# Performance work log

Measured on AMD Instinct MI355X. Metric: run time of the kernel, lower is better.

Reference implementation:

```python
import jax, jax.numpy as jnp
import numpy as np

B, N, DIM = 4, 2048, 128
HEADS, HEAD = 8, 128
INNER = HEADS * HEAD  # 1024
EPS = 1e-5


def setup_inputs() -> dict:
    key = jax.random.key(0)
    k0, k1, k2 = jax.random.split(key, 3)
    return {
        "x": jax.random.normal(k0, (B, N, DIM), jnp.float32),
        "ln_gamma": jnp.ones((DIM,), jnp.float32),
        "ln_beta": jnp.zeros((DIM,), jnp.float32),
        "w_qkv": jax.random.normal(k1, (3 * INNER, DIM), jnp.float32) * (DIM ** -0.5),
        "w_out": jax.random.normal(k2, (DIM, INNER), jnp.float32) * (INNER ** -0.5),
        "b_out": jnp.zeros((DIM,), jnp.float32),
    }


def _rope(t):
    """lucidrains-style rotary embedding over full last dim of t: [b,h,n,d]."""
    n, d = t.shape[-2], t.shape[-1]
    inv_freq = 1.0 / (10000.0 ** (jnp.arange(0, d, 2, dtype=jnp.float32) / d))
    freqs = jnp.arange(n, dtype=jnp.float32)[:, None] * inv_freq[None, :]  # [n, d/2]
    freqs = jnp.repeat(freqs, 2, axis=-1)  # interleaved duplicate -> [n, d]
    cos, sin = jnp.cos(freqs), jnp.sin(freqs)
    # rotate_half on interleaved pairs: (x1, x2) -> (-x2, x1)
    x1, x2 = t[..., 0::2], t[..., 1::2]
    rot = jnp.stack((-x2, x1), axis=-1).reshape(t.shape)
    return t * cos + rot * sin


def reference(x, ln_gamma, ln_beta, w_qkv, w_out, b_out):
    # LayerNorm
    mu = x.mean(-1, keepdims=True)
    var = x.var(-1, keepdims=True)
    xn = (x - mu) * jax.lax.rsqrt(var + EPS) * ln_gamma + ln_beta
    # QKV projection (bias-free)
    qkv = jnp.einsum('bnd,ed->bne', xn, w_qkv)  # [B, N, 3*INNER]
    q, k, v = jnp.split(qkv, 3, axis=-1)
    to_heads = lambda t: t.reshape(B, N, HEADS, HEAD).transpose(0, 2, 1, 3)
    q, k, v = to_heads(q), to_heads(k), to_heads(v)  # [B, H, N, HEAD]
    # Partial RoPE: rotate all but the last token; last token stays unrotated
    q = jnp.concatenate([_rope(q[:, :, :-1]), q[:, :, -1:]], axis=2)
    k = jnp.concatenate([_rope(k[:, :, :-1]), k[:, :, -1:]], axis=2)
    scale = HEAD ** -0.5
    dots = jnp.einsum('bhid,bhjd->bhij', q, k) * scale  # [B, H, N, N]
    attn = jax.nn.softmax(dots, axis=-1)
    out = jnp.einsum('bhij,bhjd->bhid', attn, v)
    out = out.transpose(0, 2, 1, 3).reshape(B, N, INNER)
    return out @ w_out.T + b_out
```

## Files before the change

kernel.cpp:

```cpp
#include <hip/hip_runtime.h>
#include <hip/hip_bf16.h>
#include <hip/hip_fp16.h>

#define B_      4
#define N_      2048
#define DIM_    128
#define HEADS_  8
#define HEAD_   128
#define INNER_  1024
#define QKV_    3072
#define EPS_    1e-5f
#define SCALE_  0.08838834764831845f
#define ROPE_C  0.20762050593046015f

typedef __attribute__((ext_vector_type(8))) short short8;
typedef __attribute__((ext_vector_type(4))) short short4v;
typedef __attribute__((ext_vector_type(4))) float f32x4;


__device__ __forceinline__ unsigned short f2bf(float f) {
    unsigned u = __builtin_bit_cast(unsigned, f);
    u = (u + 0x7fffu + ((u >> 16) & 1u)) >> 16;
    return (unsigned short)u;
}
__device__ __forceinline__ float bf2f(unsigned short h) {
    unsigned u = ((unsigned)h) << 16;
    return __builtin_bit_cast(float, u);
}
__device__ __forceinline__ unsigned pk2(float a, float b) {
    return (unsigned)f2bf(a) | ((unsigned)f2bf(b) << 16);
}
__device__ __forceinline__ short4v pack4(const float* e) {
    __hip_bfloat162 h0 = __float22bfloat162_rn(make_float2(e[0], e[1]));
    __hip_bfloat162 h1 = __float22bfloat162_rn(make_float2(e[2], e[3]));
    uint2 u;
    __builtin_memcpy(&u.x, &h0, 4);
    __builtin_memcpy(&u.y, &h1, 4);
    return __builtin_bit_cast(short4v, u);
}

__device__ __forceinline__ int kidx(int r, int chunk) {
    return r * 128 + ((chunk ^ (r & 7)) << 3);
}
__device__ __forceinline__ int vidx(int r, int chunk) {
    return r * 64 + ((chunk ^ (r & 7)) << 3);
}

__global__ __launch_bounds__(256) void k_ln(
    const float* __restrict__ x, const float* __restrict__ g,
    const float* __restrict__ be, unsigned short* __restrict__ xnb)
{
    const int w = threadIdx.x >> 6, l = threadIdx.x & 63;
    const int row = blockIdx.x * 4 + w;
    float2 v = *(const float2*)(x + (size_t)row * 128 + l * 2);
    float s = v.x + v.y, s2 = v.x * v.x + v.y * v.y;
#pragma unroll
    for (int off = 1; off < 64; off <<= 1) {
        s  += __shfl_xor(s, off);
        s2 += __shfl_xor(s2, off);
    }
    float mu = s * (1.f / 128.f);
    float var = s2 * (1.f / 128.f) - mu * mu;
    float rs = rsqrtf(var + EPS_);
    float2 gg = *(const float2*)(g + l * 2);
    float2 bb = *(const float2*)(be + l * 2);
    float ox = (v.x - mu) * rs * gg.x + bb.x;
    float oy = (v.y - mu) * rs * gg.y + bb.y;
    *(unsigned*)(xnb + (size_t)row * 128 + l * 2) = pk2(ox, oy);
}

__global__ __launch_bounds__(256) void k_cvt(
    const float* __restrict__ src, unsigned short* __restrict__ dst)
{
    size_t i = ((size_t)blockIdx.x * 256 + threadIdx.x) * 8;
    float4 f0 = *(const float4*)(src + i), f1 = *(const float4*)(src + i + 4);
    uint4 u = { pk2(f0.x, f0.y), pk2(f0.z, f0.w), pk2(f1.x, f1.y), pk2(f1.z, f1.w) };
    *(uint4*)(dst + i) = u;
}

__global__ __launch_bounds__(256) void k_qkvf(
    const unsigned short* __restrict__ xnb, const unsigned short* __restrict__ wb,
    unsigned short* __restrict__ Q, unsigned short* __restrict__ K,
    unsigned short* __restrict__ Vt)
{
    __shared__ unsigned short lA[128 * 136];
    __shared__ unsigned short lB[128 * 136];
    const int t = threadIdx.x;
    const int wv = t >> 6, l = t & 63;
    const int lm = l & 15, quad = l >> 4;
    const int row0 = blockIdx.x * 128;
    const int by   = blockIdx.y;
    const int e0   = by * 128;

#pragma unroll
    for (int i = 0; i < 8; ++i) {
        int c = t + 256 * i;  int r = c >> 4, c8 = c & 15;
        *(uint4*)&lA[r * 136 + c8 * 8] =
            *(const uint4*)(xnb + (size_t)(row0 + r) * 128 + c8 * 8);
        *(uint4*)&lB[r * 136 + c8 * 8] =
            *(const uint4*)(wb + (size_t)(e0 + r) * 128 + c8 * 8);
    }
    __syncthreads();

    short8 af[2][4];
#pragma unroll
    for (int mt = 0; mt < 2; ++mt)
#pragma unroll
        for (int ks = 0; ks < 4; ++ks)
            af[mt][ks] = *(short8*)&lA[(wv * 32 + mt * 16 + lm) * 136 + ks * 32 + quad * 8];

    f32x4 acc[2][8];
#pragma unroll
    for (int mt = 0; mt < 2; ++mt)
#pragma unroll
        for (int ct = 0; ct < 8; ++ct) acc[mt][ct] = (f32x4){0.f, 0.f, 0.f, 0.f};
#pragma unroll
    for (int ks = 0; ks < 4; ++ks) {
#pragma unroll
        for (int ct = 0; ct < 8; ++ct) {
            short8 b = *(short8*)&lB[(ct * 16 + lm) * 136 + ks * 32 + quad * 8];
            acc[0][ct] = __builtin_amdgcn_mfma_f32_16x16x32_bf16(af[0][ks], b, acc[0][ct], 0, 0, 0);
            acc[1][ct] = __builtin_amdgcn_mfma_f32_16x16x32_bf16(af[1][ks], b, acc[1][ct], 0, 0, 0);
        }
    }
    __syncthreads();

    const int b  = row0 >> 11;
    const int n0 = row0 & (N_ - 1);
    const int h  = by & 7;
    const int bh = b * 8 + h;

    if (by < 16) {
#pragma unroll
        for (int mt = 0; mt < 2; ++mt)
#pragma unroll
            for (int ct = 0; ct < 8; ++ct)
#pragma unroll
                for (int r = 0; r < 4; ++r)
                    lA[(wv * 32 + mt * 16 + quad * 4 + r) * 136 + ct * 16 + lm] =
                        f2bf(acc[mt][ct][r]);
        __syncthreads();

        const int r_loc = t >> 1, half = t & 1;
        const int n = n0 + r_loc;
        unsigned short* dst = (by < 8 ? Q : K) +
            ((size_t)bh * N_ + n) * HEAD_ + half * 64;
        const bool dorope = (n != N_ - 1);
#pragma unroll
        for (int j = 0; j < 8; ++j) {
            short8 vv = *(short8*)&lA[r_loc * 136 + half * 64 + j * 8];
            if (dorope) {
                unsigned short* pv = (unsigned short*)&vv;
#pragma unroll
                for (int p = 0; p < 4; ++p) {
                    int i0 = half * 32 + j * 4 + p;
                    float invf = exp2f(-(float)i0 * ROPE_C);
                    float th = (float)n * invf;
                    float cs = __cosf(th), sn = __sinf(th);
                    float e = bf2f(pv[2 * p]), o = bf2f(pv[2 * p + 1]);
                    pv[2 * p]     = f2bf(e * cs - o * sn);
                    pv[2 * p + 1] = f2bf(o * cs + e * sn);
                }
            }
            *(short8*)(dst + j * 8) = vv;
        }
    } else {
#pragma unroll
        for (int mt = 0; mt < 2; ++mt)
#pragma unroll
            for (int ct = 0; ct < 8; ++ct)
#pragma unroll
                for (int r = 0; r < 4; ++r)
                    lA[(ct * 16 + lm) * 136 + wv * 32 + quad * 8 + mt * 4 + r] =
                        f2bf(acc[mt][ct][r]);
        __syncthreads();

        const int d = t >> 1, half = t & 1;
        unsigned short* dst = Vt + ((size_t)bh * HEAD_ + d) * N_ + n0 + half * 64;
#pragma unroll
        for (int j = 0; j < 8; ++j)
            *(short8*)(dst + j * 8) = *(short8*)&lA[d * 136 + half * 64 + j * 8];
    }
}

__global__ __launch_bounds__(256) void k_attn(
    const unsigned short* __restrict__ Q, const unsigned short* __restrict__ K,
    const unsigned short* __restrict__ Vt, unsigned short* __restrict__ Ob)
{
    __shared__ unsigned short lK[64 * 128];
    __shared__ unsigned short lV[128 * 64];

    const int t = threadIdx.x;
    const int w = t >> 6, l = t & 63;
    const int lm = l & 15, quad = l >> 4;
    const int bid = blockIdx.x;
    const int bh = bid & 31;
    const int qt = bid >> 5;
    const int n0 = qt * 128;
    const unsigned short* Qb = Q  + (size_t)bh * N_ * HEAD_;
    const unsigned short* Kb = K  + (size_t)bh * N_ * HEAD_;
    const unsigned short* Vb = Vt + (size_t)bh * N_ * HEAD_;

    short8 aq[2][4];
#pragma unroll
    for (int tt = 0; tt < 2; ++tt) {
        const unsigned short* qp =
            Qb + ((size_t)(n0 + tt * 64 + w * 16 + lm)) * 128 + quad * 8;
#pragma unroll
        for (int ks = 0; ks < 4; ++ks)
            aq[tt][ks] = *(const short8*)(qp + ks * 32);
    }

    f32x4 Oa[2][8];
#pragma unroll
    for (int tt = 0; tt < 2; ++tt)
#pragma unroll
        for (int i = 0; i < 8; ++i) Oa[tt][i] = (f32x4){0.f, 0.f, 0.f, 0.f};
    float ps0 = 0.f, ps1 = 0.f;
    const float C1 = SCALE_ * 1.44269504f;
    const float C0 = -23.08312f;

    short8 kr[4], vr[4];
#pragma unroll
    for (int i = 0; i < 4; ++i) {
        int c = t + 256 * i;
        kr[i] = *(const short8*)(Kb + ((size_t)(c >> 4)) * 128 + (c & 15) * 8);
        vr[i] = *(const short8*)(Vb + (size_t)(c >> 3) * N_ + (c & 7) * 8);
    }

    for (int jt = 0; jt < 32; ++jt) {
        __syncthreads();
#pragma unroll
        for (int i = 0; i < 4; ++i) {
            int c = t + 256 * i;
            *(short8*)&lK[kidx(c >> 4, c & 15)] = kr[i];
            *(short8*)&lV[vidx(c >> 3, c & 7)]  = vr[i];
        }
        __syncthreads();
        if (jt < 31) {
#pragma unroll
            for (int i = 0; i < 4; ++i) {
                int c = t + 256 * i;
                kr[i] = *(const short8*)(Kb + ((size_t)((jt + 1) * 64 + (c >> 4))) * 128 + (c & 15) * 8);
                vr[i] = *(const short8*)(Vb + (size_t)(c >> 3) * N_ + (jt + 1) * 64 + (c & 7) * 8);
            }
        }

        short4v pf0[4], pf1[4];
#pragma unroll
        for (int nb = 0; nb < 4; ++nb) {
            f32x4 st0 = (f32x4){0.f, 0.f, 0.f, 0.f};
            f32x4 st1 = (f32x4){0.f, 0.f, 0.f, 0.f};
#pragma unroll
            for (int ks = 0; ks < 4; ++ks) {
                short8 kf = *(short8*)&lK[kidx(nb * 16 + lm, (ks << 2) + quad)];
                st0 = __builtin_amdgcn_mfma_f32_16x16x32_bf16(kf, aq[0][ks], st0, 0, 0, 0);
                st1 = __builtin_amdgcn_mfma_f32_16x16x32_bf16(kf, aq[1][ks], st1, 0, 0, 0);
            }
            float e0[4], e1[4];
#pragma unroll
            for (int r = 0; r < 4; ++r) {
                e0[r] = exp2f(st0[r] * C1 + C0);
                e1[r] = exp2f(st1[r] * C1 + C0);
                ps0 += e0[r];  ps1 += e1[r];
            }
            pf0[nb] = pack4(e0);
            pf1[nb] = pack4(e1);
        }

#pragma unroll
        for (int c2 = 0; c2 < 2; ++c2) {
            short8 ap0 = __builtin_shufflevector(pf0[2 * c2], pf0[2 * c2 + 1],
                                                 0, 1, 2, 3, 4, 5, 6, 7);
            short8 ap1 = __builtin_shufflevector(pf1[2 * c2], pf1[2 * c2 + 1],
                                                 0, 1, 2, 3, 4, 5, 6, 7);
#pragma unroll
            for (int nb8 = 0; nb8 < 8; ++nb8) {
                short8 bv = *(short8*)&lV[vidx(nb8 * 16 + lm, (c2 << 2) + quad)];
                Oa[0][nb8] = __builtin_amdgcn_mfma_f32_16x16x32_bf16(ap0, bv, Oa[0][nb8], 0, 0, 0);
                Oa[1][nb8] = __builtin_amdgcn_mfma_f32_16x16x32_bf16(ap1, bv, Oa[1][nb8], 0, 0, 0);
            }
        }
    }

    ps0 += __shfl_xor(ps0, 16);  ps0 += __shfl_xor(ps0, 32);
    ps1 += __shfl_xor(ps1, 16);  ps1 += __shfl_xor(ps1, 32);

    const int b = bh >> 3, h = bh & 7;
#pragma unroll
    for (int tt = 0; tt < 2; ++tt)
#pragma unroll
        for (int r = 0; r < 4; ++r) {
            float lsum = __shfl(tt == 0 ? ps0 : ps1, (l & 48) | (quad * 4 + r));
            float il = 1.f / lsum;
            int n = n0 + tt * 64 + w * 16 + quad * 4 + r;
            unsigned short* op = Ob + ((size_t)b * N_ + n) * INNER_ + h * HEAD_ + lm;
#pragma unroll
            for (int nb8 = 0; nb8 < 8; ++nb8)
                op[nb8 * 16] = f2bf(Oa[tt][nb8][r] * il);
        }
}

__global__ __launch_bounds__(256) void k_attn2(
    const unsigned short* __restrict__ Q, const unsigned short* __restrict__ K,
    const unsigned short* __restrict__ Vt, float* __restrict__ Opart,
    float* __restrict__ psb)
{
    __shared__ unsigned short lK[64 * 128];
    __shared__ unsigned short lV[128 * 64];

    const int t = threadIdx.x;
    const int w = t >> 6, l = t & 63;
    const int lm = l & 15, quad = l >> 4;
    const int bid = blockIdx.x;
    const int s   = bid >> 9;
    const int p   = bid & 511;
    const int bh  = bid & 31;
    const int qt  = (bid >> 5) & 15;
    const int n0  = qt * 128;
    const int jt0 = s * 16;
    const unsigned short* Qb = Q  + (size_t)bh * N_ * HEAD_;
    const unsigned short* Kb = K  + (size_t)bh * N_ * HEAD_;
    const unsigned short* Vb = Vt + (size_t)bh * N_ * HEAD_;

    short8 aq[2][4];
#pragma unroll
    for (int tt = 0; tt < 2; ++tt) {
        const unsigned short* qp =
            Qb + ((size_t)(n0 + tt * 64 + w * 16 + lm)) * 128 + quad * 8;
#pragma unroll
        for (int ks = 0; ks < 4; ++ks)
            aq[tt][ks] = *(const short8*)(qp + ks * 32);
    }

    f32x4 Oa[2][8];
#pragma unroll
    for (int tt = 0; tt < 2; ++tt)
#pragma unroll
        for (int i = 0; i < 8; ++i) Oa[tt][i] = (f32x4){0.f, 0.f, 0.f, 0.f};
    float ps0 = 0.f, ps1 = 0.f;
    const float C1 = SCALE_ * 1.44269504f;
    const float C0 = -23.08312f;

    short8 kr[4], vr[4];
#pragma unroll
    for (int i = 0; i < 4; ++i) {
        int c = t + 256 * i;
        kr[i] = *(const short8*)(Kb + ((size_t)(jt0 * 64 + (c >> 4))) * 128 + (c & 15) * 8);
        vr[i] = *(const short8*)(Vb + (size_t)(c >> 3) * N_ + jt0 * 64 + (c & 7) * 8);
    }

    for (int jt = 0; jt < 16; ++jt) {
        __syncthreads();
#pragma unroll
        for (int i = 0; i < 4; ++i) {
            int c = t + 256 * i;
            *(short8*)&lK[kidx(c >> 4, c & 15)] = kr[i];
            *(short8*)&lV[vidx(c >> 3, c & 7)]  = vr[i];
        }
        __syncthreads();
        if (jt < 15) {
#pragma unroll
            for (int i = 0; i < 4; ++i) {
                int c = t + 256 * i;
                kr[i] = *(const short8*)(Kb + ((size_t)((jt0 + jt + 1) * 64 + (c >> 4))) * 128 + (c & 15) * 8);
                vr[i] = *(const short8*)(Vb + (size_t)(c >> 3) * N_ + (jt0 + jt + 1) * 64 + (c & 7) * 8);
            }
        }

        short4v pf0[4], pf1[4];
#pragma unroll
        for (int nb = 0; nb < 4; ++nb) {
            f32x4 st0 = (f32x4){0.f, 0.f, 0.f, 0.f};
            f32x4 st1 = (f32x4){0.f, 0.f, 0.f, 0.f};
#pragma unroll
            for (int ks = 0; ks < 4; ++ks) {
                short8 kf = *(short8*)&lK[kidx(nb * 16 + lm, (ks << 2) + quad)];
                st0 = __builtin_amdgcn_mfma_f32_16x16x32_bf16(kf, aq[0][ks], st0, 0, 0, 0);
                st1 = __builtin_amdgcn_mfma_f32_16x16x32_bf16(kf, aq[1][ks], st1, 0, 0, 0);
            }
            float e0[4], e1[4];
#pragma unroll
            for (int r = 0; r < 4; ++r) {
                e0[r] = exp2f(st0[r] * C1 + C0);
                e1[r] = exp2f(st1[r] * C1 + C0);
                ps0 += e0[r];  ps1 += e1[r];
            }
            pf0[nb] = pack4(e0);
            pf1[nb] = pack4(e1);
        }

#pragma unroll
        for (int c2 = 0; c2 < 2; ++c2) {
            short8 ap0 = __builtin_shufflevector(pf0[2 * c2], pf0[2 * c2 + 1],
                                                 0, 1, 2, 3, 4, 5, 6, 7);
            short8 ap1 = __builtin_shufflevector(pf1[2 * c2], pf1[2 * c2 + 1],
                                                 0, 1, 2, 3, 4, 5, 6, 7);
#pragma unroll
            for (int nb8 = 0; nb8 < 8; ++nb8) {
                short8 bv = *(short8*)&lV[vidx(nb8 * 16 + lm, (c2 << 2) + quad)];
                Oa[0][nb8] = __builtin_amdgcn_mfma_f32_16x16x32_bf16(ap0, bv, Oa[0][nb8], 0, 0, 0);
                Oa[1][nb8] = __builtin_amdgcn_mfma_f32_16x16x32_bf16(ap1, bv, Oa[1][nb8], 0, 0, 0);
            }
        }
    }

    ps0 += __shfl_xor(ps0, 16);  ps0 += __shfl_xor(ps0, 32);
    ps1 += __shfl_xor(ps1, 16);  ps1 += __shfl_xor(ps1, 32);

    float* Op = Opart + ((size_t)(s * 512 + p)) * 16384;
    float* pp = psb   + ((size_t)(s * 512 + p)) * 128;
#pragma unroll
    for (int tt = 0; tt < 2; ++tt)
#pragma unroll
        for (int r = 0; r < 4; ++r) {
            float lsum = __shfl(tt == 0 ? ps0 : ps1, (l & 48) | (quad * 4 + r));
            int rowl = tt * 64 + w * 16 + quad * 4 + r;
            if (lm == 0) pp[rowl] = lsum;
#pragma unroll
            for (int nb8 = 0; nb8 < 8; ++nb8)
                Op[rowl * 128 + nb8 * 16 + lm] = Oa[tt][nb8][r];
        }
}

__global__ __launch_bounds__(256) void k_comb(
    const float* __restrict__ Opart, const float* __restrict__ psb,
    unsigned short* __restrict__ Ob)
{
    __shared__ float inv[128];
    const int p = blockIdx.x;
    const int t = threadIdx.x;
    const int bh = p & 31, qt = p >> 5;
    if (t < 128) {
        float d = psb[(size_t)p * 128 + t] + psb[(size_t)(512 + p) * 128 + t];
        inv[t] = 1.f / d;
    }
    __syncthreads();
    const float* O0 = Opart + (size_t)p * 16384;
    const float* O1 = Opart + (size_t)(512 + p) * 16384;
    const int b = bh >> 3, h = bh & 7;
#pragma unroll
    for (int i = 0; i < 16; ++i) {
        int flat = i * 256 + t;
        int row = flat >> 5, dq = (flat & 31) * 4;
        float4 a = *(const float4*)(O0 + row * 128 + dq);
        float4 c = *(const float4*)(O1 + row * 128 + dq);
        float iv = inv[row];
        float e[4] = { (a.x + c.x) * iv, (a.y + c.y) * iv,
                       (a.z + c.z) * iv, (a.w + c.w) * iv };
        short4v o = pack4(e);
        int n = qt * 128 + row;
        *(short4v*)(Ob + ((size_t)b * N_ + n) * INNER_ + h * HEAD_ + dq) = o;
    }
}

__global__ __launch_bounds__(256) void k_proj(
    const unsigned short* __restrict__ Ob, const unsigned short* __restrict__ wob,
    const float* __restrict__ bias, float* __restrict__ out)
{
    __shared__ unsigned short lA[64 * 136];
    __shared__ unsigned short lB[64 * 136];
    float* lCf = (float*)lA;
    const int t = threadIdx.x;
    const int wv = t >> 6, l = t & 63;
    const int lm = l & 15, quad = l >> 4;
    const int row0 = blockIdx.x * 64;
    const int e0   = blockIdx.y * 64;

    f32x4 acc[4];
#pragma unroll
    for (int ct = 0; ct < 4; ++ct) acc[ct] = (f32x4){0.f, 0.f, 0.f, 0.f};

    for (int kt = 0; kt < 8; ++kt) {
        __syncthreads();
#pragma unroll
        for (int i = 0; i < 4; ++i) {
            int c = t + 256 * i;  int r = c >> 4, c8 = c & 15;
            *(uint4*)&lA[r * 136 + c8 * 8] =
                *(const uint4*)(Ob + (size_t)(row0 + r) * 1024 + kt * 128 + c8 * 8);
            *(uint4*)&lB[r * 136 + c8 * 8] =
                *(const uint4*)(wob + (size_t)(e0 + r) * 1024 + kt * 128 + c8 * 8);
        }
        __syncthreads();
        short8 a_[4];
#pragma unroll
        for (int ks = 0; ks < 4; ++ks)
            a_[ks] = *(short8*)&lA[(wv * 16 + lm) * 136 + ks * 32 + quad * 8];
#pragma unroll
        for (int ks = 0; ks < 4; ++ks)
#pragma unroll
            for (int ct = 0; ct < 4; ++ct) {
                short8 b = *(short8*)&lB[(ct * 16 + lm) * 136 + ks * 32 + quad * 8];
                acc[ct] = __builtin_amdgcn_mfma_f32_16x16x32_bf16(a_[ks], b, acc[ct], 0, 0, 0);
            }
    }
    __syncthreads();
#pragma unroll
    for (int ct = 0; ct < 4; ++ct)
#pragma unroll
        for (int r = 0; r < 4; ++r)
            lCf[(wv * 16 + quad * 4 + r) * 68 + ct * 16 + lm] = acc[ct][r];
    __syncthreads();
#pragma unroll
    for (int i = 0; i < 4; ++i) {
        int c = t + 256 * i;  int r = c >> 4, c4 = c & 15;
        float4 v = *(float4*)&lCf[r * 68 + c4 * 4];
        float4 b4 = *(const float4*)(bias + e0 + c4 * 4);
        v.x += b4.x; v.y += b4.y; v.z += b4.z; v.w += b4.w;
        *(float4*)(out + (size_t)(row0 + r) * 128 + e0 + c4 * 4) = v;
    }
}

extern "C" void kernel_launch(void* const* d_in, const int* in_sizes, int n_in,
                              void* d_out, int out_size, void* d_ws, size_t ws_size,
                              hipStream_t stream) {
    const float* x      = (const float*)d_in[0];
    const float* gamma  = (const float*)d_in[1];
    const float* beta   = (const float*)d_in[2];
    const float* w_qkv  = (const float*)d_in[3];
    const float* w_out  = (const float*)d_in[4];
    const float* b_out  = (const float*)d_in[5];
    float* out = (float*)d_out;
    char* wsb = (char*)d_ws;
    unsigned short* Q    = (unsigned short*)(wsb);
    unsigned short* K    = (unsigned short*)(wsb + (16ull << 20));
    unsigned short* Vt   = (unsigned short*)(wsb + (32ull << 20));
    unsigned short* Ob   = (unsigned short*)(wsb + (48ull << 20));
    unsigned short* xnb  = (unsigned short*)(wsb + (96ull << 20));
    unsigned short* wqb  = (unsigned short*)(wsb + (98ull << 20));
    unsigned short* wob  = (unsigned short*)(wsb + (99ull << 20));

    k_ln       <<<dim3(2048),    256, 0, stream>>>(x, gamma, beta, xnb);
    k_cvt      <<<dim3(192),     256, 0, stream>>>(w_qkv, wqb);
    k_cvt      <<<dim3(64),      256, 0, stream>>>(w_out, wob);
    k_qkvf     <<<dim3(64, 24),  256, 0, stream>>>(xnb, wqb, Q, K, Vt);

    if (ws_size >= (165ull << 20)) {
        float* Opart = (float*)(wsb + (100ull << 20));
        float* psb   = (float*)(wsb + (164ull << 20));
        k_attn2 <<<dim3(1024), 256, 0, stream>>>(Q, K, Vt, Opart, psb);
        k_comb  <<<dim3(512),  256, 0, stream>>>(Opart, psb, Ob);
    } else {
        k_attn  <<<dim3(512),  256, 0, stream>>>(Q, K, Vt, Ob);
    }
    k_proj     <<<dim3(128, 2),  256, 0, stream>>>(Ob, wob, b_out, out);
}
```

Baseline: 208.1 us.

## Fuse prep kernels, shrink qkv LDS, retile projection, add attn2 occupancy hint

```diff
diff --git a/kernel.cpp b/kernel.cpp
--- a/kernel.cpp
+++ b/kernel.cpp
@@ -46,36 +46,42 @@
     return r * 64 + ((chunk ^ (r & 7)) << 3);
 }
 
-__global__ __launch_bounds__(256) void k_ln(
+__global__ __launch_bounds__(256) void k_prep(
     const float* __restrict__ x, const float* __restrict__ g,
-    const float* __restrict__ be, unsigned short* __restrict__ xnb)
+    const float* __restrict__ be, const float* __restrict__ w_qkv,
+    const float* __restrict__ w_out, unsigned short* __restrict__ xnb,
+    unsigned short* __restrict__ wqb, unsigned short* __restrict__ wob)
 {
-    const int w = threadIdx.x >> 6, l = threadIdx.x & 63;
-    const int row = blockIdx.x * 4 + w;
-    float2 v = *(const float2*)(x + (size_t)row * 128 + l * 2);
-    float s = v.x + v.y, s2 = v.x * v.x + v.y * v.y;
-#pragma unroll
-    for (int off = 1; off < 64; off <<= 1) {
-        s  += __shfl_xor(s, off);
-        s2 += __shfl_xor(s2, off);
-    }
-    float mu = s * (1.f / 128.f);
-    float var = s2 * (1.f / 128.f) - mu * mu;
-    float rs = rsqrtf(var + EPS_);
-    float2 gg = *(const float2*)(g + l * 2);
-    float2 bb = *(const float2*)(be + l * 2);
-    float ox = (v.x - mu) * rs * gg.x + bb.x;
-    float oy = (v.y - mu) * rs * gg.y + bb.y;
-    *(unsigned*)(xnb + (size_t)row * 128 + l * 2) = pk2(ox, oy);
-}
-
-__global__ __launch_bounds__(256) void k_cvt(
-    const float* __restrict__ src, unsigned short* __restrict__ dst)
-{
-    size_t i = ((size_t)blockIdx.x * 256 + threadIdx.x) * 8;
-    float4 f0 = *(const float4*)(src + i), f1 = *(const float4*)(src + i + 4);
-    uint4 u = { pk2(f0.x, f0.y), pk2(f0.z, f0.w), pk2(f1.x, f1.y), pk2(f1.z, f1.w) };
-    *(uint4*)(dst + i) = u;
+    const int bid = blockIdx.x;
+    if (bid < 2048) {
+        const int w = threadIdx.x >> 6, l = threadIdx.x & 63;
+        const int row = bid * 4 + w;
+        float2 v = *(const float2*)(x + (size_t)row * 128 + l * 2);
+        float s = v.x + v.y, s2 = v.x * v.x + v.y * v.y;
+#pragma unroll
+        for (int off = 1; off < 64; off <<= 1) {
+            s  += __shfl_xor(s, off);
+            s2 += __shfl_xor(s2, off);
+        }
+        float mu = s * (1.f / 128.f);
+        float var = s2 * (1.f / 128.f) - mu * mu;
+        float rs = rsqrtf(var + EPS_);
+        float2 gg = *(const float2*)(g + l * 2);
+        float2 bb = *(const float2*)(be + l * 2);
+        float ox = (v.x - mu) * rs * gg.x + bb.x;
+        float oy = (v.y - mu) * rs * gg.y + bb.y;
+        *(unsigned*)(xnb + (size_t)row * 128 + l * 2) = pk2(ox, oy);
+    } else if (bid < 2240) {
+        size_t i = ((size_t)(bid - 2048) * 256 + threadIdx.x) * 8;
+        float4 f0 = *(const float4*)(w_qkv + i), f1 = *(const float4*)(w_qkv + i + 4);
+        uint4 u = { pk2(f0.x, f0.y), pk2(f0.z, f0.w), pk2(f1.x, f1.y), pk2(f1.z, f1.w) };
+        *(uint4*)(wqb + i) = u;
+    } else {
+        size_t i = ((size_t)(bid - 2240) * 256 + threadIdx.x) * 8;
+        float4 f0 = *(const float4*)(w_out + i), f1 = *(const float4*)(w_out + i + 4);
+        uint4 u = { pk2(f0.x, f0.y), pk2(f0.z, f0.w), pk2(f1.x, f1.y), pk2(f1.z, f1.w) };
+        *(uint4*)(wob + i) = u;
+    }
 }
 
 __global__ __launch_bounds__(256) void k_qkvf(
@@ -83,8 +89,7 @@
     unsigned short* __restrict__ Q, unsigned short* __restrict__ K,
     unsigned short* __restrict__ Vt)
 {
-    __shared__ unsigned short lA[128 * 136];
-    __shared__ unsigned short lB[128 * 136];
+    __shared__ unsigned short lB[128 * 128];
     const int t = threadIdx.x;
     const int wv = t >> 6, l = t & 63;
     const int lm = l & 15, quad = l >> 4;
@@ -92,33 +97,33 @@
     const int by   = blockIdx.y;
     const int e0   = by * 128;
 
+    short8 af[2][4];
+#pragma unroll
+    for (int mt = 0; mt < 2; ++mt)
+#pragma unroll
+        for (int ks = 0; ks < 4; ++ks)
+            af[mt][ks] = *(const short8*)(
+                xnb + (size_t)(row0 + wv * 32 + mt * 16 + lm) * 128 + ks * 32 + quad * 8);
+
 #pragma unroll
     for (int i = 0; i < 8; ++i) {
         int c = t + 256 * i;  int r = c >> 4, c8 = c & 15;
-        *(uint4*)&lA[r * 136 + c8 * 8] =
-            *(const uint4*)(xnb + (size_t)(row0 + r) * 128 + c8 * 8);
-        *(uint4*)&lB[r * 136 + c8 * 8] =
+        *(uint4*)&lB[r * 128 + ((c8 ^ (r & 7)) << 3)] =
             *(const uint4*)(wb + (size_t)(e0 + r) * 128 + c8 * 8);
     }
     __syncthreads();
 
-    short8 af[2][4];
+    f32x4 acc[2][8];
 #pragma unroll
     for (int mt = 0; mt < 2; ++mt)
 #pragma unroll
-        for (int ks = 0; ks < 4; ++ks)
-            af[mt][ks] = *(short8*)&lA[(wv * 32 + mt * 16 + lm) * 136 + ks * 32 + quad * 8];
-
-    f32x4 acc[2][8];
-#pragma unroll
-    for (int mt = 0; mt < 2; ++mt)
-#pragma unroll
         for (int ct = 0; ct < 8; ++ct) acc[mt][ct] = (f32x4){0.f, 0.f, 0.f, 0.f};
 #pragma unroll
     for (int ks = 0; ks < 4; ++ks) {
 #pragma unroll
         for (int ct = 0; ct < 8; ++ct) {
-            short8 b = *(short8*)&lB[(ct * 16 + lm) * 136 + ks * 32 + quad * 8];
+            int r = ct * 16 + lm;
+            short8 b = *(short8*)&lB[r * 128 + (((ks * 4 + quad) ^ (r & 7)) << 3)];
             acc[0][ct] = __builtin_amdgcn_mfma_f32_16x16x32_bf16(af[0][ks], b, acc[0][ct], 0, 0, 0);
             acc[1][ct] = __builtin_amdgcn_mfma_f32_16x16x32_bf16(af[1][ks], b, acc[1][ct], 0, 0, 0);
         }
@@ -136,9 +141,12 @@
 #pragma unroll
             for (int ct = 0; ct < 8; ++ct)
 #pragma unroll
-                for (int r = 0; r < 4; ++r)
-                    lA[(wv * 32 + mt * 16 + quad * 4 + r) * 136 + ct * 16 + lm] =
+                for (int r = 0; r < 4; ++r) {
+                    int row = wv * 32 + mt * 16 + quad * 4 + r;
+                    int chunk = ct * 2 + (lm >> 3);
+                    lB[row * 128 + ((chunk ^ (row & 7)) << 3) + (lm & 7)] =
                         f2bf(acc[mt][ct][r]);
+                }
         __syncthreads();
 
         const int r_loc = t >> 1, half = t & 1;
@@ -148,7 +156,7 @@
         const bool dorope = (n != N_ - 1);
 #pragma unroll
         for (int j = 0; j < 8; ++j) {
-            short8 vv = *(short8*)&lA[r_loc * 136 + half * 64 + j * 8];
+            short8 vv = *(short8*)&lB[r_loc * 128 + (((half * 8 + j) ^ (r_loc & 7)) << 3)];
             if (dorope) {
                 unsigned short* pv = (unsigned short*)&vv;
 #pragma unroll
@@ -170,16 +178,20 @@
 #pragma unroll
             for (int ct = 0; ct < 8; ++ct)
 #pragma unroll
-                for (int r = 0; r < 4; ++r)
-                    lA[(ct * 16 + lm) * 136 + wv * 32 + quad * 8 + mt * 4 + r] =
+                for (int r = 0; r < 4; ++r) {
+                    int row = ct * 16 + lm;
+                    int chunk = wv * 4 + quad;
+                    lB[row * 128 + ((chunk ^ (row & 7)) << 3) + mt * 4 + r] =
                         f2bf(acc[mt][ct][r]);
+                }
         __syncthreads();
 
         const int d = t >> 1, half = t & 1;
         unsigned short* dst = Vt + ((size_t)bh * HEAD_ + d) * N_ + n0 + half * 64;
 #pragma unroll
         for (int j = 0; j < 8; ++j)
-            *(short8*)(dst + j * 8) = *(short8*)&lA[d * 136 + half * 64 + j * 8];
+            *(short8*)(dst + j * 8) =
+                *(short8*)&lB[d * 128 + (((half * 8 + j) ^ (d & 7)) << 3)];
     }
 }
 
@@ -187,8 +199,8 @@
     const unsigned short* __restrict__ Q, const unsigned short* __restrict__ K,
     const unsigned short* __restrict__ Vt, unsigned short* __restrict__ Ob)
 {
-    __shared__ unsigned short lK[64 * 128];
-    __shared__ unsigned short lV[128 * 64];
+    __shared__ unsigned short lK[64 * 136];
+    __shared__ unsigned short lV[128 * 68];
 
     const int t = threadIdx.x;
     const int w = t >> 6, l = t & 63;
@@ -233,8 +245,8 @@
 #pragma unroll
         for (int i = 0; i < 4; ++i) {
             int c = t + 256 * i;
-            *(short8*)&lK[kidx(c >> 4, c & 15)] = kr[i];
-            *(short8*)&lV[vidx(c >> 3, c & 7)]  = vr[i];
+            *(short8*)&lK[(c >> 4) * 136 + (c & 15) * 8] = kr[i];
+            *(short8*)&lV[(c >> 3) * 68  + (c & 7)  * 8] = vr[i];
         }
         __syncthreads();
         if (jt < 31) {
@@ -253,7 +265,7 @@
             f32x4 st1 = (f32x4){0.f, 0.f, 0.f, 0.f};
 #pragma unroll
             for (int ks = 0; ks < 4; ++ks) {
-                short8 kf = *(short8*)&lK[kidx(nb * 16 + lm, (ks << 2) + quad)];
+                short8 kf = *(short8*)&lK[(nb * 16 + lm) * 136 + ks * 32 + quad * 8];
                 st0 = __builtin_amdgcn_mfma_f32_16x16x32_bf16(kf, aq[0][ks], st0, 0, 0, 0);
                 st1 = __builtin_amdgcn_mfma_f32_16x16x32_bf16(kf, aq[1][ks], st1, 0, 0, 0);
             }
@@ -276,7 +288,7 @@
                                                  0, 1, 2, 3, 4, 5, 6, 7);
 #pragma unroll
             for (int nb8 = 0; nb8 < 8; ++nb8) {
-                short8 bv = *(short8*)&lV[vidx(nb8 * 16 + lm, (c2 << 2) + quad)];
+                short8 bv = *(short8*)&lV[(nb8 * 16 + lm) * 68 + c2 * 32 + quad * 8];
                 Oa[0][nb8] = __builtin_amdgcn_mfma_f32_16x16x32_bf16(ap0, bv, Oa[0][nb8], 0, 0, 0);
                 Oa[1][nb8] = __builtin_amdgcn_mfma_f32_16x16x32_bf16(ap1, bv, Oa[1][nb8], 0, 0, 0);
             }
@@ -301,7 +313,7 @@
         }
 }
 
-__global__ __launch_bounds__(256) void k_attn2(
+__global__ __launch_bounds__(256, 3) void k_attn2(
     const unsigned short* __restrict__ Q, const unsigned short* __restrict__ K,
     const unsigned short* __restrict__ Vt, float* __restrict__ Opart,
     float* __restrict__ psb)
@@ -458,26 +470,31 @@
     const unsigned short* __restrict__ Ob, const unsigned short* __restrict__ wob,
     const float* __restrict__ bias, float* __restrict__ out)
 {
-    __shared__ unsigned short lA[64 * 136];
+    __shared__ unsigned short lA[32 * 136];
     __shared__ unsigned short lB[64 * 136];
     float* lCf = (float*)lA;
     const int t = threadIdx.x;
     const int wv = t >> 6, l = t & 63;
     const int lm = l & 15, quad = l >> 4;
-    const int row0 = blockIdx.x * 64;
+    const int rt = wv & 1, ch = wv >> 1;
+    const int row0 = blockIdx.x * 32;
     const int e0   = blockIdx.y * 64;
 
-    f32x4 acc[4];
-#pragma unroll
-    for (int ct = 0; ct < 4; ++ct) acc[ct] = (f32x4){0.f, 0.f, 0.f, 0.f};
+    f32x4 acc[2];
+#pragma unroll
+    for (int ct = 0; ct < 2; ++ct) acc[ct] = (f32x4){0.f, 0.f, 0.f, 0.f};
 
     for (int kt = 0; kt < 8; ++kt) {
         __syncthreads();
 #pragma unroll
-        for (int i = 0; i < 4; ++i) {
+        for (int i = 0; i < 2; ++i) {
             int c = t + 256 * i;  int r = c >> 4, c8 = c & 15;
             *(uint4*)&lA[r * 136 + c8 * 8] =
                 *(const uint4*)(Ob + (size_t)(row0 + r) * 1024 + kt * 128 + c8 * 8);
+        }
+#pragma unroll
+        for (int i = 0; i < 4; ++i) {
+            int c = t + 256 * i;  int r = c >> 4, c8 = c & 15;
             *(uint4*)&lB[r * 136 + c8 * 8] =
                 *(const uint4*)(wob + (size_t)(e0 + r) * 1024 + kt * 128 + c8 * 8);
         }
@@ -485,24 +502,24 @@
         short8 a_[4];
 #pragma unroll
         for (int ks = 0; ks < 4; ++ks)
-            a_[ks] = *(short8*)&lA[(wv * 16 + lm) * 136 + ks * 32 + quad * 8];
+            a_[ks] = *(short8*)&lA[(rt * 16 + lm) * 136 + ks * 32 + quad * 8];
 #pragma unroll
         for (int ks = 0; ks < 4; ++ks)
 #pragma unroll
-            for (int ct = 0; ct < 4; ++ct) {
-                short8 b = *(short8*)&lB[(ct * 16 + lm) * 136 + ks * 32 + quad * 8];
+            for (int ct = 0; ct < 2; ++ct) {
+                short8 b = *(short8*)&lB[(ch * 32 + ct * 16 + lm) * 136 + ks * 32 + quad * 8];
                 acc[ct] = __builtin_amdgcn_mfma_f32_16x16x32_bf16(a_[ks], b, acc[ct], 0, 0, 0);
             }
     }
     __syncthreads();
 #pragma unroll
-    for (int ct = 0; ct < 4; ++ct)
+    for (int ct = 0; ct < 2; ++ct)
 #pragma unroll
         for (int r = 0; r < 4; ++r)
-            lCf[(wv * 16 + quad * 4 + r) * 68 + ct * 16 + lm] = acc[ct][r];
+            lCf[(rt * 16 + quad * 4 + r) * 68 + ch * 32 + ct * 16 + lm] = acc[ct][r];
     __syncthreads();
 #pragma unroll
-    for (int i = 0; i < 4; ++i) {
+    for (int i = 0; i < 2; ++i) {
         int c = t + 256 * i;  int r = c >> 4, c4 = c & 15;
         float4 v = *(float4*)&lCf[r * 68 + c4 * 4];
         float4 b4 = *(const float4*)(bias + e0 + c4 * 4);
@@ -530,10 +547,9 @@
     unsigned short* wqb  = (unsigned short*)(wsb + (98ull << 20));
     unsigned short* wob  = (unsigned short*)(wsb + (99ull << 20));
 
-    k_ln       <<<dim3(2048),    256, 0, stream>>>(x, gamma, beta, xnb);
-    k_cvt      <<<dim3(192),     256, 0, stream>>>(w_qkv, wqb);
-    k_cvt      <<<dim3(64),      256, 0, stream>>>(w_out, wob);
-    k_qkvf     <<<dim3(64, 24),  256, 0, stream>>>(xnb, wqb, Q, K, Vt);
+    k_prep <<<dim3(2304),    256, 0, stream>>>(x, gamma, beta, w_qkv, w_out,
+                                               xnb, wqb, wob);
+    k_qkvf <<<dim3(64, 24),  256, 0, stream>>>(xnb, wqb, Q, K, Vt);
 
     if (ws_size >= (165ull << 20)) {
         float* Opart = (float*)(wsb + (100ull << 20));
@@ -543,5 +559,5 @@
     } else {
         k_attn  <<<dim3(512),  256, 0, stream>>>(Q, K, Vt, Ob);
     }
-    k_proj     <<<dim3(128, 2),  256, 0, stream>>>(Ob, wob, b_out, out);
-}
+    k_proj <<<dim3(256, 2),  256, 0, stream>>>(Ob, wob, b_out, out);
+}
```

Result: no change. 207.7 us (-0.2%).
